# Performance work log

Measured on AMD Instinct MI355X. Metric: run time of the kernel, lower is better.

The kernel has to match this reference:

```python
import jax, jax.numpy as jnp
import numpy as np

B, NE, NN, L = 64, 256, 1024, 512
F_IN, HID = 128, 128
VOCAB = 50000
ALPHA = 0.2
NEG = -9.0e15


def _leaky(z):
    return jnp.where(z >= 0, z, ALPHA * z)


def hga_layer(x, adj, W, W2, W3, a, a2, wc, transfer, concat):
    # x: [B, NN, Fin], adj: [B, NE, NN] (hyperedge incidence)
    O = W2.shape[1]
    x4 = x @ W2                      # [B, NN, O]
    if transfer:
        x = x @ W                    # [B, NN, O]
    # node->edge attention: score depends only on node k (query is shared word_context)
    s0 = wc[0] @ a[:O, 0]            # scalar
    e1 = _leaky(x4 @ a[O:, 0] + s0)  # [B, NN]
    e1 = jnp.broadcast_to(e1[:, None, :], adj.shape)          # [B, NE, NN]
    att_edge = jax.nn.softmax(jnp.where(adj > 0, e1, NEG), axis=2)
    edge = att_edge @ x              # [B, NE, O]
    edge4 = edge @ W3                # [B, NE, O]
    # edge->node attention: query = node feat x4[k], key = edge feat edge4[j]
    e2 = _leaky((x4 @ a2[:O, 0])[:, None, :] + (edge4 @ a2[O:, 0])[:, :, None])  # [B, NE, NN]
    att_node = jax.nn.softmax(jnp.where(adj > 0, e2, NEG).transpose(0, 2, 1), axis=2)  # [B, NN, NE]
    node = att_node @ edge           # [B, NN, O]
    return jax.nn.elu(node) if concat else node


def setup_inputs() -> dict:
    key = jax.random.key(0)
    ks = jax.random.split(key, 16)
    stdv = 1.0 / np.sqrt(HID)
    u = lambda k, shape: jax.random.uniform(k, shape, jnp.float32, -stdv, stdv)
    inp = {
        "items": jax.random.randint(ks[0], (B, NN), 0, VOCAB),
        "alias_inputs": jax.random.randint(ks[1], (B, L), 0, NN),
        "node_masks": jnp.ones((B, L), jnp.float32),
        "adj": jax.random.randint(ks[2], (B, NE, NN), 0, 2).astype(jnp.float32),
        "emb": jax.random.normal(ks[3], (VOCAB, F_IN), jnp.float32),
        # layer 1 (transfer=False, concat=True)
        "w2_1": u(ks[4], (F_IN, HID)),
        "w3_1": u(ks[5], (HID, HID)),
        "a_1": u(ks[6], (2 * HID, 1)),
        "a2_1": u(ks[7], (2 * HID, 1)),
        "wc_1": u(ks[8], (1, HID)),
        # layer 2 (transfer=True, concat=False)
        "w_2": u(ks[9], (HID, HID)),
        "w2_2": u(ks[10], (HID, HID)),
        "w3_2": u(ks[11], (HID, HID)),
        "a_2": u(ks[12], (2 * HID, 1)),
        "a2_2": u(ks[13], (2 * HID, 1)),
        "wc_2": u(ks[14], (1, HID)),
        "ln_g": jnp.ones((HID,), jnp.float32),
        "ln_b": jnp.zeros((HID,), jnp.float32),
    }
    return inp


def reference(items, alias_inputs, node_masks, adj, emb,
              w2_1, w3_1, a_1, a2_1, wc_1,
              w_2, w2_2, w3_2, a_2, a2_2, wc_2,
              ln_g, ln_b):
    hidden = emb[items]                                        # [B, NN, F]
    x = hga_layer(hidden, adj, None, w2_1, w3_1, a_1, a2_1, wc_1,
                  transfer=False, concat=True)
    x = hga_layer(x, adj, w_2, w2_2, w3_2, a_2, a2_2, wc_2,
                  transfer=True, concat=False)                 # [B, NN, HID]
    seq = jnp.take_along_axis(x, alias_inputs[:, :, None], axis=1)  # [B, L, HID]
    m = node_masks[:, :, None]
    h = seq * m
    b = jnp.sum(h * m, axis=-2) / jnp.sum(node_masks, -1, keepdims=True)  # [B, HID]
    mu = jnp.mean(b, -1, keepdims=True)
    var = jnp.mean((b - mu) ** 2, -1, keepdims=True)
    return (b - mu) / jnp.sqrt(var + 1e-6) * ln_g + ln_b
```

## Files before the change

kernel.cpp:

```cpp
#include <hip/hip_runtime.h>
#include <hip/hip_bf16.h>

typedef __hip_bfloat16 bf16;
typedef __attribute__((ext_vector_type(8))) unsigned short u16x8;
typedef __attribute__((ext_vector_type(4))) unsigned short u16x4;
typedef __attribute__((ext_vector_type(4))) float f32x4;
typedef __attribute__((ext_vector_type(8))) short bf16x8;

#define B_   64
#define NE_  256
#define NN_  1024
#define L_   512
#define HID_ 128
#define ALPHA_ 0.2f

__device__ __forceinline__ float bfu(unsigned short u){
  unsigned int x = ((unsigned int)u) << 16;
  union { unsigned int i; float f; } c; c.i = x; return c.f;
}
__device__ __forceinline__ unsigned short f2b(float f){
  bf16 h = __float2bfloat16(f);
  union { bf16 b; unsigned short u; } c; c.b = h; return c.u;
}
__device__ __forceinline__ int swz(int r, int c){ return (c ^ (r & 3) ^ ((r >> 2) & 3)) & 3; }

__global__ void k_small(const float* __restrict__ w2_1, const float* __restrict__ w3_1,
                        const float* __restrict__ a_1,  const float* __restrict__ a2_1,
                        const float* __restrict__ wc_1,
                        const float* __restrict__ w2_2, const float* __restrict__ w3_2,
                        const float* __restrict__ a_2,  const float* __restrict__ a2_2,
                        const float* __restrict__ wc_2,
                        const float* __restrict__ w_2,
                        const int* __restrict__ alias, const float* __restrict__ masks,
                        float* __restrict__ consts, unsigned short* __restrict__ W2T,
                        float* __restrict__ wcount, float* __restrict__ msum,
                        float* __restrict__ pooled)
{
  __shared__ float wcs[1024];
  __shared__ float red4[4];
  int blk = blockIdx.x, t = threadIdx.x;
  if (blk < 6) {
    if (t < 128) {
      const float* M; const float* v;
      switch (blk) {
        case 0: M = w2_1; v = a_1  + 128; break;
        case 1: M = w2_1; v = a2_1;       break;
        case 2: M = w3_1; v = a2_1 + 128; break;
        case 3: M = w2_2; v = a_2  + 128; break;
        case 4: M = w2_2; v = a2_2;       break;
        default: M = w3_2; v = a2_2 + 128; break;
      }
      float acc = 0.f;
      #pragma unroll 4
      for (int o = 0; o < 128; o += 4) {
        f32x4 m = *(const f32x4*)(M + t*128 + o);
        f32x4 x = *(const f32x4*)(v + o);
        acc += m[0]*x[0] + m[1]*x[1] + m[2]*x[2] + m[3]*x[3];
      }
      consts[blk*128 + t] = acc;
    }
  } else if (blk < 8) {
    const float* wc = (blk == 6) ? wc_1 : wc_2;
    const float* a  = (blk == 6) ? a_1  : a_2;
    if (t < 64) {
      float s = wc[t]*a[t] + wc[t+64]*a[t+64];
      #pragma unroll
      for (int sh = 32; sh > 0; sh >>= 1) s += __shfl_xor(s, sh);
      if (t == 0) consts[768 + (blk - 6)] = s;
    }
  } else if (blk == 8) {
    if (t < 128) for (int k = 0; k < 128; ++k) W2T[t*128 + k] = f2b(w_2[k*128 + t]);
  } else if (blk == 9) {
    for (int i = t; i < B_*HID_; i += 256) pooled[i] = 0.f;
  } else {
    int b = blk - 10;
    #pragma unroll
    for (int j = 0; j < 4; ++j) wcs[t + j*256] = 0.f;
    __syncthreads();
    float s = 0.f;
    #pragma unroll
    for (int j = 0; j < 2; ++j) {
      int l = t + j*256;
      float m = masks[b*L_ + l];
      int idx = alias[b*L_ + l];
      atomicAdd(&wcs[idx], m*m);
      s += m;
    }
    #pragma unroll
    for (int sh = 32; sh > 0; sh >>= 1) s += __shfl_xor(s, sh);
    if ((t & 63) == 0) red4[t >> 6] = s;
    __syncthreads();
    if (t == 0) msum[b] = red4[0] + red4[1] + red4[2] + red4[3];
    #pragma unroll
    for (int j = 0; j < 4; ++j) wcount[(long)b*NN_ + t + j*256] = wcs[t + j*256];
  }
}

__global__ __launch_bounds__(256) void k_prep(
    const float* __restrict__ adj,
    unsigned long long* __restrict__ ADJBb,
    unsigned short* __restrict__ ADJT16)
{
  __shared__ unsigned long long Lbits[16][17];
  const int id = blockIdx.x;
  const int b  = id & 63;
  const int ec = id >> 6;
  const int t  = threadIdx.x;
  const int r  = t >> 4;
  const int c  = t & 15;
  const int e  = ec*16 + r;
  const float* src = adj + ((long)b*NE_ + e)*NN_ + c*64;
  unsigned long long m = 0;
  #pragma unroll
  for (int j = 0; j < 64; j += 4) {
    f32x4 v = *(const f32x4*)(src + j);
    #pragma unroll
    for (int k = 0; k < 4; ++k)
      m |= (unsigned long long)(v[k] != 0.f) << (j + k);
  }
  ADJBb[((long)b*NE_ + e)*16 + c] = m;
  Lbits[r][c] = m;
  __syncthreads();
  #pragma unroll
  for (int j = 0; j < 4; ++j) {
    int n = t + 256*j;
    int w = n >> 6, bitn = n & 63;
    unsigned int o = 0;
    #pragma unroll
    for (int rr = 0; rr < 16; ++rr)
      o |= (unsigned int)((Lbits[rr][w] >> bitn) & 1ull) << rr;
    ADJT16[((long)b*NN_ + n)*16 + ec] = (unsigned short)o;
  }
}

__global__ void k_fproj(const float* __restrict__ emb, const int* __restrict__ gitems,
                        const float* __restrict__ consts,
                        float* __restrict__ w1, float* __restrict__ f1,
                        unsigned short* __restrict__ YT)
{
  __shared__ float ce1s[128], cf1s[128];
  __shared__ __attribute__((aligned(16))) unsigned short T[64][132];
  int b = blockIdx.y, n0 = blockIdx.x * 64, t = threadIdx.x;
  if (t < 128) { ce1s[t] = consts[t]; cf1s[t] = consts[128 + t]; }
  __syncthreads();
  int r = t >> 2, h0 = (t & 3) * 32;
  long row = (long)b*NN_ + n0 + r;
  float s0 = consts[768];
  float xv[32];
  const float* sp = emb + (long)gitems[row]*HID_ + h0;
  #pragma unroll
  for (int j = 0; j < 32; j += 4) {
    f32x4 v = *(const f32x4*)(sp + j);
    #pragma unroll
    for (int k = 0; k < 4; ++k) xv[j+k] = v[k];
  }
  float p1 = 0.f, p2 = 0.f;
  #pragma unroll
  for (int j = 0; j < 32; ++j) { p1 += xv[j]*ce1s[h0+j]; p2 += xv[j]*cf1s[h0+j]; }
  p1 += __shfl_xor(p1, 1, 4); p1 += __shfl_xor(p1, 2, 4);
  p2 += __shfl_xor(p2, 1, 4); p2 += __shfl_xor(p2, 2, 4);
  float z = p1 + s0; z = (z >= 0.f) ? z : ALPHA_*z;
  float w = __expf(z);
  if ((t & 3) == 0) { w1[row] = w; f1[row] = p2; }
  #pragma unroll
  for (int j = 0; j < 32; j += 4) {
    u16x4 o;
    #pragma unroll
    for (int k = 0; k < 4; ++k) o[k] = f2b(w * xv[j+k]);
    *(u16x4*)&T[r][h0+j] = o;
  }
  __syncthreads();
  int h = t >> 1, nh = (t & 1) * 32;
  unsigned short* dst = YT + ((long)b*HID_ + h)*NN_ + n0 + nh;
  #pragma unroll
  for (int j = 0; j < 32; j += 8) {
    u16x8 o;
    #pragma unroll
    for (int k = 0; k < 8; ++k) o[k] = T[nh+j+k][h];
    *(u16x8*)&dst[j] = o;
  }
}

template<int TRANSFER>
__global__ __launch_bounds__(256) void k_gemm_edge(
    const unsigned char* __restrict__ ADJ8,
    const unsigned short* __restrict__ YT,
    const float* __restrict__ w1v,
    const float* __restrict__ consts, int layer,
    const unsigned short* __restrict__ W2T,
    unsigned short* __restrict__ ET,
    float* __restrict__ f2o)
{
  __shared__ __attribute__((aligned(16))) unsigned short SM[12288];
  __shared__ float dsum[64];
  const int id = blockIdx.x;
  const int b = id & 63;
  const long e0 = (long)(id >> 6) * 64;
  const int t = threadIdx.x;
  const int lane = t & 63;
  const int w = t >> 6, wm = w >> 1, wn = w & 1;
  const int r4 = t >> 2, c4 = t & 3;
  const int lr = lane & 15, g = lane >> 4;

  f32x4 acc[2][4];
  #pragma unroll
  for (int i = 0; i < 2; ++i)
    #pragma unroll
    for (int j = 0; j < 4; ++j) acc[i][j] = (f32x4){0.f,0.f,0.f,0.f};

  const unsigned char*  Ab = ADJ8 + ((long)b*NE_ + e0 + r4)*(NN_ >> 3);
  const unsigned short* Bb = YT + (long)b*HID_*NN_;
  const float*          wb = w1v + (long)b*NN_;

  unsigned int ab; u16x8 bv0, bv1; f32x4 wv0, wv1;
  float dot = 0.f;

  auto stage = [&](int kc) {
    ab  = Ab[(kc >> 3) + c4];
    wv0 = *(const f32x4*)(wb + kc + c4*8);
    wv1 = *(const f32x4*)(wb + kc + c4*8 + 4);
    bv0 = *(const u16x8*)(Bb + (long)r4*NN_ + kc + c4*8);
    bv1 = *(const u16x8*)(Bb + (long)(64+r4)*NN_ + kc + c4*8);
  };
  auto commit = [&](int buf) {
    u16x8 av;
    #pragma unroll
    for (int j = 0; j < 8; ++j) {
      unsigned int bit = (ab >> j) & 1u;
      av[j] = bit ? (unsigned short)0x3F80 : (unsigned short)0;
      float wj = (j < 4) ? wv0[j] : wv1[j-4];
      dot += bit ? wj : 0.f;
    }
    *(u16x8*)&SM[buf*2048 + r4*32 + swz(r4,c4)*8] = av;
    *(u16x8*)&SM[4096 + buf*4096 + r4*32 + swz(r4,c4)*8] = bv0;
    *(u16x8*)&SM[4096 + buf*4096 + (64+r4)*32 + swz(64+r4,c4)*8] = bv1;
  };

  stage(0); commit(0);
  int cur = 0;
  const int NIT = NN_/32;
  for (int it = 0; it < NIT; ++it) {
    __syncthreads();
    if (it+1 < NIT) stage((it+1)*32);
    const unsigned short* AsB = &SM[cur*2048];
    const unsigned short* BsB = &SM[4096 + cur*4096];
    bf16x8 af[2], bfr[4];
    #pragma unroll
    for (int mt = 0; mt < 2; ++mt) {
      int r = wm*32 + mt*16 + lr;
      af[mt] = *(const bf16x8*)&AsB[r*32 + swz(r,g)*8];
    }
    #pragma unroll
    for (int nt = 0; nt < 4; ++nt) {
      int n = wn*64 + nt*16 + lr;
      bfr[nt] = *(const bf16x8*)&BsB[n*32 + swz(n,g)*8];
    }
    #pragma unroll
    for (int mt = 0; mt < 2; ++mt)
      #pragma unroll
      for (int nt = 0; nt < 4; ++nt)
        acc[mt][nt] = __builtin_amdgcn_mfma_f32_16x16x32_bf16(af[mt], bfr[nt], acc[mt][nt], 0, 0, 0);
    if (it+1 < NIT) { commit(cur^1); cur ^= 1; }
  }
  dot += __shfl_down(dot, 2, 4); dot += __shfl_down(dot, 1, 4);
  if ((lane & 3) == 0) dsum[r4] = dot;
  __syncthreads();
  #pragma unroll
  for (int mt = 0; mt < 2; ++mt)
    #pragma unroll
    for (int nt = 0; nt < 4; ++nt) {
      int col = wn*64 + nt*16 + lr;
      #pragma unroll
      for (int q = 0; q < 4; ++q) {
        int rl = wm*32 + mt*16 + g*4 + q;
        SM[rl*136 + col] = f2b(acc[mt][nt][q] / dsum[rl]);
      }
    }
  __syncthreads();
  if (TRANSFER) {
    f32x4 acc2[2][4];
    #pragma unroll
    for (int i = 0; i < 2; ++i)
      #pragma unroll
      for (int j = 0; j < 4; ++j) acc2[i][j] = (f32x4){0.f,0.f,0.f,0.f};
    #pragma unroll
    for (int kc2 = 0; kc2 < 4; ++kc2) {
      bf16x8 af[2], bfr[4];
      #pragma unroll
      for (int mt = 0; mt < 2; ++mt) {
        int r = wm*32 + mt*16 + lr;
        af[mt] = *(const bf16x8*)&SM[r*136 + kc2*32 + g*8];
      }
      #pragma unroll
      for (int nt = 0; nt < 4; ++nt) {
        int n = wn*64 + nt*16 + lr;
        bfr[nt] = *(const bf16x8*)(W2T + n*128 + kc2*32 + g*8);
      }
      #pragma unroll
      for (int mt = 0; mt < 2; ++mt)
        #pragma unroll
        for (int nt = 0; nt < 4; ++nt)
          acc2[mt][nt] = __builtin_amdgcn_mfma_f32_16x16x32_bf16(af[mt], bfr[nt], acc2[mt][nt], 0, 0, 0);
    }
    __syncthreads();
    #pragma unroll
    for (int mt = 0; mt < 2; ++mt)
      #pragma unroll
      for (int nt = 0; nt < 4; ++nt) {
        int col = wn*64 + nt*16 + lr;
        #pragma unroll
        for (int q = 0; q < 4; ++q) {
          int rl = wm*32 + mt*16 + g*4 + q;
          SM[rl*136 + col] = f2b(acc2[mt][nt][q]);
        }
      }
    __syncthreads();
  }
  {
    const float* cf2 = consts + layer*384 + 256;
    int r = t >> 2, h0 = (t & 3) * 32;
    float p = 0.f;
    #pragma unroll
    for (int j = 0; j < 32; ++j) p += bfu(SM[r*136 + h0 + j]) * cf2[h0 + j];
    p += __shfl_down(p, 2, 4); p += __shfl_down(p, 1, 4);
    if ((t & 3) == 0) f2o[(long)b*NE_ + e0 + r] = p;
  }
  {
    int h = t >> 1, eh = (t & 1) * 32;
    unsigned short* dst = ET + ((long)b*HID_ + h)*NE_ + e0 + eh;
    #pragma unroll
    for (int j = 0; j < 32; j += 8) {
      u16x8 o;
      #pragma unroll
      for (int k = 0; k < 8; ++k) o[k] = SM[(eh+j+k)*136 + h];
      *(u16x8*)&dst[j] = o;
    }
  }
}

template<int EPI>
__global__ __launch_bounds__(256, 2) void k_gemm_att(
    const unsigned char* __restrict__ ADJ8,
    const unsigned short* __restrict__ ET,
    const float* __restrict__ f1v, const float* __restrict__ f2v,
    const float* __restrict__ consts,
    unsigned short* __restrict__ YTout, float* __restrict__ w1o, float* __restrict__ f1o,
    const float* __restrict__ wcount, float* __restrict__ pooled)
{
  __shared__ __attribute__((aligned(16))) unsigned short SM[12288];
  __shared__ float dsum[64];
  __shared__ float colsum[128];
  __shared__ float wrow[64];
  const int id = blockIdx.x;
  const int b = id & 63;
  const long m0 = (long)(id >> 6) * 64;
  const int t = threadIdx.x;
  const int lane = t & 63;
  const int w = t >> 6, wm = w >> 1, wn = w & 1;
  const int r4 = t >> 2, c4 = t & 3;
  const int lr = lane & 15, g = lane >> 4;

  f32x4 acc[2][4];
  #pragma unroll
  for (int i = 0; i < 2; ++i)
    #pragma unroll
    for (int j = 0; j < 4; ++j) acc[i][j] = (f32x4){0.f,0.f,0.f,0.f};

  const float f1r = f1v[(long)b*NN_ + m0 + r4];
  const unsigned char*  Ab = ADJ8 + ((long)b*NN_ + m0 + r4)*(NE_ >> 3);
  const unsigned short* Bb = ET + (long)b*HID_*NE_;
  const float* f2p = f2v + (long)b*NE_;

  unsigned int ab; u16x8 bv0, bv1; f32x4 fv0, fv1;
  float dot = 0.f;

  auto stage = [&](int kc) {
    ab  = Ab[(kc >> 3) + c4];
    fv0 = *(const f32x4*)(f2p + kc + c4*8);
    fv1 = *(const f32x4*)(f2p + kc + c4*8 + 4);
    bv0 = *(const u16x8*)(Bb + (long)r4*NE_ + kc + c4*8);
    bv1 = *(const u16x8*)(Bb + (long)(64+r4)*NE_ + kc + c4*8);
  };
  auto commit = [&](int buf) {
    u16x8 av;
    #pragma unroll
    for (int j = 0; j < 8; ++j) {
      unsigned int bit = (ab >> j) & 1u;
      float z = f1r + ((j < 4) ? fv0[j] : fv1[j-4]);
      z = (z >= 0.f) ? z : ALPHA_ * z;
      float wt = bit ? __expf(z) : 0.f;
      unsigned short us = f2b(wt);
      av[j] = us; dot += bfu(us);
    }
    *(u16x8*)&SM[buf*2048 + r4*32 + swz(r4,c4)*8] = av;
    *(u16x8*)&SM[4096 + buf*4096 + r4*32 + swz(r4,c4)*8] = bv0;
    *(u16x8*)&SM[4096 + buf*4096 + (64+r4)*32 + swz(64+r4,c4)*8] = bv1;
  };

  stage(0); commit(0);
  int cur = 0;
  const int NIT = NE_/32;
  for (int it = 0; it < NIT; ++it) {
    __syncthreads();
    if (it+1 < NIT) stage((it+1)*32);
    const unsigned short* AsB = &SM[cur*2048];
    const unsigned short* BsB = &SM[4096 + cur*4096];
    bf16x8 af[2], bfr[4];
    #pragma unroll
    for (int mt = 0; mt < 2; ++mt) {
      int r = wm*32 + mt*16 + lr;
      af[mt] = *(const bf16x8*)&AsB[r*32 + swz(r,g)*8];
    }
    #pragma unroll
    for (int nt = 0; nt < 4; ++nt) {
      int n = wn*64 + nt*16 + lr;
      bfr[nt] = *(const bf16x8*)&BsB[n*32 + swz(n,g)*8];
    }
    #pragma unroll
    for (int mt = 0; mt < 2; ++mt)
      #pragma unroll
      for (int nt = 0; nt < 4; ++nt)
        acc[mt][nt] = __builtin_amdgcn_mfma_f32_16x16x32_bf16(af[mt], bfr[nt], acc[mt][nt], 0, 0, 0);
    if (it+1 < NIT) { commit(cur^1); cur ^= 1; }
  }
  dot += __shfl_down(dot, 2, 4); dot += __shfl_down(dot, 1, 4);
  if ((lane & 3) == 0) dsum[r4] = dot;
  if (EPI == 2 && t < 128) colsum[t] = 0.f;
  __syncthreads();

  if (EPI == 1) {
    #pragma unroll
    for (int mt = 0; mt < 2; ++mt)
      #pragma unroll
      for (int nt = 0; nt < 4; ++nt) {
        int col = wn*64 + nt*16 + lr;
        #pragma unroll
        for (int q = 0; q < 4; ++q) {
          int rl = wm*32 + mt*16 + g*4 + q;
          float v = acc[mt][nt][q] / dsum[rl];
          v = (v > 0.f) ? v : expm1f(v);
          SM[rl*136 + col] = f2b(v);
        }
      }
    __syncthreads();
    {
      const float* ce1 = consts + 384;
      const float* cf1 = consts + 512;
      int r = t >> 2, h0 = (t & 3) * 32;
      float p1 = 0.f, p2 = 0.f;
      #pragma unroll
      for (int j = 0; j < 32; ++j) {
        float xv = bfu(SM[r*136 + h0 + j]);
        p1 += xv * ce1[h0 + j];
        p2 += xv * cf1[h0 + j];
      }
      p1 += __shfl_down(p1, 2, 4); p1 += __shfl_down(p1, 1, 4);
      p2 += __shfl_down(p2, 2, 4); p2 += __shfl_down(p2, 1, 4);
      if ((t & 3) == 0) {
        float z = p1 + consts[769];
        z = (z >= 0.f) ? z : ALPHA_ * z;
        float wv = __expf(z);
        wrow[r] = wv;
        w1o[(long)b*NN_ + m0 + r] = wv;
        f1o[(long)b*NN_ + m0 + r] = p2;
      }
    }
    __syncthreads();
    {
      int h = t >> 1, nh = (t & 1) * 32;
      unsigned short* dst = YTout + ((long)b*HID_ + h)*NN_ + m0 + nh;
      #pragma unroll
      for (int j = 0; j < 32; j += 8) {
        u16x8 o;
        #pragma unroll
        for (int k = 0; k < 8; ++k) {
          int rr = nh + j + k;
          o[k] = f2b(wrow[rr] * bfu(SM[rr*136 + h]));
        }
        *(u16x8*)&dst[j] = o;
      }
    }
  } else {
    float psum[4] = {0.f, 0.f, 0.f, 0.f};
    #pragma unroll
    for (int mt = 0; mt < 2; ++mt)
      #pragma unroll
      for (int q = 0; q < 4; ++q) {
        int rl = wm*32 + mt*16 + g*4 + q;
        float wc = wcount[(long)b*NN_ + m0 + rl];
        float inv = wc / dsum[rl];
        #pragma unroll
        for (int nt = 0; nt < 4; ++nt) psum[nt] += inv * acc[mt][nt][q];
      }
    #pragma unroll
    for (int nt = 0; nt < 4; ++nt) atomicAdd(&colsum[wn*64 + nt*16 + lr], psum[nt]);
    __syncthreads();
    if (t < 128) atomicAdd(&pooled[(long)b*HID_ + t], colsum[t]);
  }
}

__global__ void k_ln(const float* __restrict__ pooled, const float* __restrict__ msum,
                     const float* __restrict__ ln_g, const float* __restrict__ ln_b,
                     float* __restrict__ out)
{
  int b = blockIdx.x, t = threadIdx.x;
  __shared__ float sr[2];
  float bv = pooled[b*HID_ + t] / msum[b];
  int lane = t & 63;
  float p = bv;
  #pragma unroll
  for (int s = 32; s > 0; s >>= 1) p += __shfl_xor(p, s);
  if (lane == 0) sr[t >> 6] = p;
  __syncthreads();
  float mu = (sr[0] + sr[1]) * (1.f / HID_);
  float dv = bv - mu;
  p = dv * dv;
  #pragma unroll
  for (int s = 32; s > 0; s >>= 1) p += __shfl_xor(p, s);
  __syncthreads();
  if (lane == 0) sr[t >> 6] = p;
  __syncthreads();
  float var = (sr[0] + sr[1]) * (1.f / HID_);
  out[b*HID_ + t] = dv / sqrtf(var + 1e-6f) * ln_g[t] + ln_b[t];
}

extern "C" void kernel_launch(void* const* d_in, const int* in_sizes, int n_in,
                              void* d_out, int out_size, void* d_ws, size_t ws_size,
                              hipStream_t stream)
{
  const int*   items = (const int*)d_in[0];
  const int*   alias = (const int*)d_in[1];
  const float* masks = (const float*)d_in[2];
  const float* adj   = (const float*)d_in[3];
  const float* emb   = (const float*)d_in[4];
  const float* w2_1  = (const float*)d_in[5];
  const float* w3_1  = (const float*)d_in[6];
  const float* a_1   = (const float*)d_in[7];
  const float* a2_1  = (const float*)d_in[8];
  const float* wc_1  = (const float*)d_in[9];
  const float* w_2   = (const float*)d_in[10];
  const float* w2_2  = (const float*)d_in[11];
  const float* w3_2  = (const float*)d_in[12];
  const float* a_2   = (const float*)d_in[13];
  const float* a2_2  = (const float*)d_in[14];
  const float* wc_2  = (const float*)d_in[15];
  const float* ln_g  = (const float*)d_in[16];
  const float* ln_b  = (const float*)d_in[17];
  float* out = (float*)d_out;

  char* ws = (char*)d_ws;
  size_t off = 0;
  auto alloc = [&](size_t bytes) -> void* {
    void* p = ws + off; off += (bytes + 255) / 256 * 256; return p;
  };
  unsigned long long* ADJBb = (unsigned long long*)alloc((size_t)B_*NE_*(NN_/8));
  unsigned short*     ADJT16= (unsigned short*)    alloc((size_t)B_*NN_*(NE_/8));
  unsigned short* YT   = (unsigned short*)alloc((size_t)B_*HID_*NN_*2);
  unsigned short* ET   = (unsigned short*)alloc((size_t)B_*HID_*NE_*2);
  float* wcount= (float*)alloc((size_t)B_*NN_*4);
  float* pooled= (float*)alloc((size_t)B_*HID_*4);
  float* w1L1  = (float*)alloc((size_t)B_*NN_*4);
  float* f1L1  = (float*)alloc((size_t)B_*NN_*4);
  float* w1L2  = (float*)alloc((size_t)B_*NN_*4);
  float* f1L2  = (float*)alloc((size_t)B_*NN_*4);
  float* f2    = (float*)alloc((size_t)B_*NE_*4);
  float* msum  = (float*)alloc(B_*4);
  float* consts= (float*)alloc(772*4);
  unsigned short* W2T = (unsigned short*)alloc((size_t)HID_*HID_*2);
  if (off > ws_size) return;

  k_small<<<74, 256, 0, stream>>>(w2_1, w3_1, a_1, a2_1, wc_1, w2_2, w3_2, a_2, a2_2, wc_2,
                                  w_2, alias, masks, consts, W2T, wcount, msum, pooled);
  k_prep<<<B_*16, 256, 0, stream>>>(adj, ADJBb, ADJT16);
  k_fproj<<<dim3(NN_/64, B_), 256, 0, stream>>>(emb, items, consts, w1L1, f1L1, YT);

  k_gemm_edge<0><<<B_*(NE_/64), 256, 0, stream>>>((const unsigned char*)ADJBb, YT, w1L1,
        consts, 0, W2T, ET, f2);
  k_gemm_att<1><<<B_*(NN_/64), 256, 0, stream>>>((const unsigned char*)ADJT16, ET, f1L1, f2,
        consts, YT, w1L2, f1L2, nullptr, nullptr);

  k_gemm_edge<1><<<B_*(NE_/64), 256, 0, stream>>>((const unsigned char*)ADJBb, YT, w1L2,
        consts, 1, W2T, ET, f2);
  k_gemm_att<2><<<B_*(NN_/64), 256, 0, stream>>>((const unsigned char*)ADJT16, ET, f1L2, f2,
        consts, nullptr, nullptr, nullptr, wcount, pooled);

  k_ln<<<B_, HID_, 0, stream>>>(pooled, msum, ln_g, ln_b, out);
}
```

Measured before the change: 130.2 us.

## Split-K edge GEMM with combine kernel and fuse front-end kernels

Merges the small-constant, adjacency bit-packing and feature-projection kernels into one launch. The feature-projection blocks recompute their projection constants locally, so they no longer depend on the constants kernel. The node->edge GEMM is split over two halves of the node dimension, doubling its grid from 256 to 512 blocks to fill more CUs. A new combine kernel sums the fp32 partials and denominators, normalizes, and applies the W transfer and f2 epilogue. This costs fp32 partial-result traffic through global memory and extra launches.

Result: slower. 136.9 us (+5.2%).

```diff
diff --git a/kernel.cpp b/kernel.cpp
--- a/kernel.cpp
+++ b/kernel.cpp
@@ -13,6 +13,7 @@
 #define L_   512
 #define HID_ 128
 #define ALPHA_ 0.2f
+#define PSC_ ((long)B_*NE_*HID_)
 
 __device__ __forceinline__ float bfu(unsigned short u){
   unsigned int x = ((unsigned int)u) << 16;
@@ -24,178 +25,194 @@
 }
 __device__ __forceinline__ int swz(int r, int c){ return (c ^ (r & 3) ^ ((r >> 2) & 3)) & 3; }
 
-__global__ void k_small(const float* __restrict__ w2_1, const float* __restrict__ w3_1,
-                        const float* __restrict__ a_1,  const float* __restrict__ a2_1,
-                        const float* __restrict__ wc_1,
-                        const float* __restrict__ w2_2, const float* __restrict__ w3_2,
-                        const float* __restrict__ a_2,  const float* __restrict__ a2_2,
-                        const float* __restrict__ wc_2,
-                        const float* __restrict__ w_2,
-                        const int* __restrict__ alias, const float* __restrict__ masks,
-                        float* __restrict__ consts, unsigned short* __restrict__ W2T,
-                        float* __restrict__ wcount, float* __restrict__ msum,
-                        float* __restrict__ pooled)
+__global__ __launch_bounds__(256) void k_front(
+    const float* __restrict__ adj,
+    unsigned long long* __restrict__ ADJBb, unsigned short* __restrict__ ADJT16,
+    const float* __restrict__ emb, const int* __restrict__ items,
+    const float* __restrict__ w2_1, const float* __restrict__ w3_1,
+    const float* __restrict__ a_1,  const float* __restrict__ a2_1,
+    const float* __restrict__ wc_1,
+    const float* __restrict__ w_2,
+    const float* __restrict__ w2_2, const float* __restrict__ w3_2,
+    const float* __restrict__ a_2,  const float* __restrict__ a2_2,
+    const float* __restrict__ wc_2,
+    const int* __restrict__ alias, const float* __restrict__ masks,
+    float* __restrict__ w1L1, float* __restrict__ f1L1,
+    unsigned short* __restrict__ YT,
+    float* __restrict__ consts, unsigned short* __restrict__ W2T,
+    float* __restrict__ wcount, float* __restrict__ msum, float* __restrict__ pooled)
 {
-  __shared__ float wcs[1024];
-  __shared__ float red4[4];
-  int blk = blockIdx.x, t = threadIdx.x;
-  if (blk < 6) {
-    if (t < 128) {
-      const float* M; const float* v;
-      switch (blk) {
-        case 0: M = w2_1; v = a_1  + 128; break;
-        case 1: M = w2_1; v = a2_1;       break;
-        case 2: M = w3_1; v = a2_1 + 128; break;
-        case 3: M = w2_2; v = a_2  + 128; break;
-        case 4: M = w2_2; v = a2_2;       break;
-        default: M = w3_2; v = a2_2 + 128; break;
-      }
+  __shared__ __attribute__((aligned(16))) unsigned char SMEM[18944];
+  const int id = blockIdx.x;
+  const int t  = threadIdx.x;
+
+  if (id < 1024) {
+    unsigned long long (*Lbits)[17] = (unsigned long long(*)[17])SMEM;
+    const int b  = id & 63;
+    const int ec = id >> 6;
+    const int r  = t >> 4;
+    const int c  = t & 15;
+    const int e  = ec*16 + r;
+    const float* src = adj + ((long)b*NE_ + e)*NN_ + c*64;
+    unsigned long long m = 0;
+    #pragma unroll
+    for (int j = 0; j < 64; j += 4) {
+      f32x4 v = *(const f32x4*)(src + j);
+      #pragma unroll
+      for (int k = 0; k < 4; ++k)
+        m |= (unsigned long long)(v[k] != 0.f) << (j + k);
+    }
+    ADJBb[((long)b*NE_ + e)*16 + c] = m;
+    Lbits[r][c] = m;
+    __syncthreads();
+    #pragma unroll
+    for (int j = 0; j < 4; ++j) {
+      int n = t + 256*j;
+      int w = n >> 6, bitn = n & 63;
+      unsigned int o = 0;
+      #pragma unroll
+      for (int rr = 0; rr < 16; ++rr)
+        o |= (unsigned int)((Lbits[rr][w] >> bitn) & 1ull) << rr;
+      ADJT16[((long)b*NN_ + n)*16 + ec] = (unsigned short)o;
+    }
+  } else if (id < 2048) {
+    float* ce1s = (float*)SMEM;
+    float* cf1s = (float*)(SMEM + 512);
+    float* s0s  = (float*)(SMEM + 1024);
+    unsigned short (*T)[132] = (unsigned short(*)[132])(SMEM + 1056);
+    {
+      int rr = t & 127;
+      const float* Mrow = w2_1 + rr*128;
+      const float* vv = (t < 128) ? (a_1 + 128) : a2_1;
       float acc = 0.f;
       #pragma unroll 4
       for (int o = 0; o < 128; o += 4) {
-        f32x4 m = *(const f32x4*)(M + t*128 + o);
-        f32x4 x = *(const f32x4*)(v + o);
+        f32x4 m = *(const f32x4*)(Mrow + o);
+        f32x4 x = *(const f32x4*)(vv + o);
         acc += m[0]*x[0] + m[1]*x[1] + m[2]*x[2] + m[3]*x[3];
       }
-      consts[blk*128 + t] = acc;
-    }
-  } else if (blk < 8) {
-    const float* wc = (blk == 6) ? wc_1 : wc_2;
-    const float* a  = (blk == 6) ? a_1  : a_2;
-    if (t < 64) {
-      float s = wc[t]*a[t] + wc[t+64]*a[t+64];
+      if (t < 128) ce1s[rr] = acc; else cf1s[rr] = acc;
+      if (t < 64) {
+        float s = wc_1[t]*a_1[t] + wc_1[t+64]*a_1[t+64];
+        #pragma unroll
+        for (int sh = 32; sh > 0; sh >>= 1) s += __shfl_xor(s, sh);
+        if (t == 0) s0s[0] = s;
+      }
+    }
+    __syncthreads();
+    int fid = id - 1024;
+    int b = fid & 63, n0 = (fid >> 6) * 64;
+    int r = t >> 2, h0 = (t & 3) * 32;
+    long row = (long)b*NN_ + n0 + r;
+    float s0 = s0s[0];
+    float xv[32];
+    const float* sp = emb + (long)items[row]*HID_ + h0;
+    #pragma unroll
+    for (int j = 0; j < 32; j += 4) {
+      f32x4 v = *(const f32x4*)(sp + j);
+      #pragma unroll
+      for (int k = 0; k < 4; ++k) xv[j+k] = v[k];
+    }
+    float p1 = 0.f, p2 = 0.f;
+    #pragma unroll
+    for (int j = 0; j < 32; ++j) { p1 += xv[j]*ce1s[h0+j]; p2 += xv[j]*cf1s[h0+j]; }
+    p1 += __shfl_xor(p1, 1, 4); p1 += __shfl_xor(p1, 2, 4);
+    p2 += __shfl_xor(p2, 1, 4); p2 += __shfl_xor(p2, 2, 4);
+    float z = p1 + s0; z = (z >= 0.f) ? z : ALPHA_*z;
+    float w = __expf(z);
+    if ((t & 3) == 0) { w1L1[row] = w; f1L1[row] = p2; }
+    #pragma unroll
+    for (int j = 0; j < 32; j += 4) {
+      u16x4 o;
+      #pragma unroll
+      for (int k = 0; k < 4; ++k) o[k] = f2b(w * xv[j+k]);
+      *(u16x4*)&T[r][h0+j] = o;
+    }
+    __syncthreads();
+    int h = t >> 1, nh = (t & 1) * 32;
+    unsigned short* dst = YT + ((long)b*HID_ + h)*NN_ + n0 + nh;
+    #pragma unroll
+    for (int j = 0; j < 32; j += 8) {
+      u16x8 o;
+      #pragma unroll
+      for (int k = 0; k < 8; ++k) o[k] = T[nh+j+k][h];
+      *(u16x8*)&dst[j] = o;
+    }
+  } else {
+    int blk = id - 2048;
+    float* wcs  = (float*)SMEM;
+    float* red4 = (float*)(SMEM + 4096);
+    if (blk < 6) {
+      if (t < 128) {
+        const float* M; const float* v;
+        switch (blk) {
+          case 0: M = w2_1; v = a_1  + 128; break;
+          case 1: M = w2_1; v = a2_1;       break;
+          case 2: M = w3_1; v = a2_1 + 128; break;
+          case 3: M = w2_2; v = a_2  + 128; break;
+          case 4: M = w2_2; v = a2_2;       break;
+          default: M = w3_2; v = a2_2 + 128; break;
+        }
+        float acc = 0.f;
+        #pragma unroll 4
+        for (int o = 0; o < 128; o += 4) {
+          f32x4 m = *(const f32x4*)(M + t*128 + o);
+          f32x4 x = *(const f32x4*)(v + o);
+          acc += m[0]*x[0] + m[1]*x[1] + m[2]*x[2] + m[3]*x[3];
+        }
+        consts[blk*128 + t] = acc;
+      }
+    } else if (blk < 8) {
+      const float* wc = (blk == 6) ? wc_1 : wc_2;
+      const float* a  = (blk == 6) ? a_1  : a_2;
+      if (t < 64) {
+        float s = wc[t]*a[t] + wc[t+64]*a[t+64];
+        #pragma unroll
+        for (int sh = 32; sh > 0; sh >>= 1) s += __shfl_xor(s, sh);
+        if (t == 0) consts[768 + (blk - 6)] = s;
+      }
+    } else if (blk == 8) {
+      if (t < 128) for (int k = 0; k < 128; ++k) W2T[t*128 + k] = f2b(w_2[k*128 + t]);
+    } else if (blk == 9) {
+      for (int i = t; i < B_*HID_; i += 256) pooled[i] = 0.f;
+    } else {
+      int b = blk - 10;
+      #pragma unroll
+      for (int j = 0; j < 4; ++j) wcs[t + j*256] = 0.f;
+      __syncthreads();
+      float s = 0.f;
+      #pragma unroll
+      for (int j = 0; j < 2; ++j) {
+        int l = t + j*256;
+        float m = masks[b*L_ + l];
+        int idx = alias[b*L_ + l];
+        atomicAdd(&wcs[idx], m*m);
+        s += m;
+      }
       #pragma unroll
       for (int sh = 32; sh > 0; sh >>= 1) s += __shfl_xor(s, sh);
-      if (t == 0) consts[768 + (blk - 6)] = s;
-    }
-  } else if (blk == 8) {
-    if (t < 128) for (int k = 0; k < 128; ++k) W2T[t*128 + k] = f2b(w_2[k*128 + t]);
-  } else if (blk == 9) {
-    for (int i = t; i < B_*HID_; i += 256) pooled[i] = 0.f;
-  } else {
-    int b = blk - 10;
-    #pragma unroll
-    for (int j = 0; j < 4; ++j) wcs[t + j*256] = 0.f;
-    __syncthreads();
-    float s = 0.f;
-    #pragma unroll
-    for (int j = 0; j < 2; ++j) {
-      int l = t + j*256;
-      float m = masks[b*L_ + l];
-      int idx = alias[b*L_ + l];
-      atomicAdd(&wcs[idx], m*m);
-      s += m;
-    }
-    #pragma unroll
-    for (int sh = 32; sh > 0; sh >>= 1) s += __shfl_xor(s, sh);
-    if ((t & 63) == 0) red4[t >> 6] = s;
-    __syncthreads();
-    if (t == 0) msum[b] = red4[0] + red4[1] + red4[2] + red4[3];
-    #pragma unroll
-    for (int j = 0; j < 4; ++j) wcount[(long)b*NN_ + t + j*256] = wcs[t + j*256];
-  }
-}
-
-__global__ __launch_bounds__(256) void k_prep(
-    const float* __restrict__ adj,
-    unsigned long long* __restrict__ ADJBb,
-    unsigned short* __restrict__ ADJT16)
-{
-  __shared__ unsigned long long Lbits[16][17];
-  const int id = blockIdx.x;
-  const int b  = id & 63;
-  const int ec = id >> 6;
-  const int t  = threadIdx.x;
-  const int r  = t >> 4;
-  const int c  = t & 15;
-  const int e  = ec*16 + r;
-  const float* src = adj + ((long)b*NE_ + e)*NN_ + c*64;
-  unsigned long long m = 0;
-  #pragma unroll
-  for (int j = 0; j < 64; j += 4) {
-    f32x4 v = *(const f32x4*)(src + j);
-    #pragma unroll
-    for (int k = 0; k < 4; ++k)
-      m |= (unsigned long long)(v[k] != 0.f) << (j + k);
-  }
-  ADJBb[((long)b*NE_ + e)*16 + c] = m;
-  Lbits[r][c] = m;
-  __syncthreads();
-  #pragma unroll
-  for (int j = 0; j < 4; ++j) {
-    int n = t + 256*j;
-    int w = n >> 6, bitn = n & 63;
-    unsigned int o = 0;
-    #pragma unroll
-    for (int rr = 0; rr < 16; ++rr)
-      o |= (unsigned int)((Lbits[rr][w] >> bitn) & 1ull) << rr;
-    ADJT16[((long)b*NN_ + n)*16 + ec] = (unsigned short)o;
-  }
-}
-
-__global__ void k_fproj(const float* __restrict__ emb, const int* __restrict__ gitems,
-                        const float* __restrict__ consts,
-                        float* __restrict__ w1, float* __restrict__ f1,
-                        unsigned short* __restrict__ YT)
-{
-  __shared__ float ce1s[128], cf1s[128];
-  __shared__ __attribute__((aligned(16))) unsigned short T[64][132];
-  int b = blockIdx.y, n0 = blockIdx.x * 64, t = threadIdx.x;
-  if (t < 128) { ce1s[t] = consts[t]; cf1s[t] = consts[128 + t]; }
-  __syncthreads();
-  int r = t >> 2, h0 = (t & 3) * 32;
-  long row = (long)b*NN_ + n0 + r;
-  float s0 = consts[768];
-  float xv[32];
-  const float* sp = emb + (long)gitems[row]*HID_ + h0;
-  #pragma unroll
-  for (int j = 0; j < 32; j += 4) {
-    f32x4 v = *(const f32x4*)(sp + j);
-    #pragma unroll
-    for (int k = 0; k < 4; ++k) xv[j+k] = v[k];
-  }
-  float p1 = 0.f, p2 = 0.f;
-  #pragma unroll
-  for (int j = 0; j < 32; ++j) { p1 += xv[j]*ce1s[h0+j]; p2 += xv[j]*cf1s[h0+j]; }
-  p1 += __shfl_xor(p1, 1, 4); p1 += __shfl_xor(p1, 2, 4);
-  p2 += __shfl_xor(p2, 1, 4); p2 += __shfl_xor(p2, 2, 4);
-  float z = p1 + s0; z = (z >= 0.f) ? z : ALPHA_*z;
-  float w = __expf(z);
-  if ((t & 3) == 0) { w1[row] = w; f1[row] = p2; }
-  #pragma unroll
-  for (int j = 0; j < 32; j += 4) {
-    u16x4 o;
-    #pragma unroll
-    for (int k = 0; k < 4; ++k) o[k] = f2b(w * xv[j+k]);
-    *(u16x4*)&T[r][h0+j] = o;
-  }
-  __syncthreads();
-  int h = t >> 1, nh = (t & 1) * 32;
-  unsigned short* dst = YT + ((long)b*HID_ + h)*NN_ + n0 + nh;
-  #pragma unroll
-  for (int j = 0; j < 32; j += 8) {
-    u16x8 o;
-    #pragma unroll
-    for (int k = 0; k < 8; ++k) o[k] = T[nh+j+k][h];
-    *(u16x8*)&dst[j] = o;
-  }
-}
-
-template<int TRANSFER>
-__global__ __launch_bounds__(256) void k_gemm_edge(
+      if ((t & 63) == 0) red4[t >> 6] = s;
+      __syncthreads();
+      if (t == 0) msum[b] = red4[0] + red4[1] + red4[2] + red4[3];
+      #pragma unroll
+      for (int j = 0; j < 4; ++j) wcount[(long)b*NN_ + t + j*256] = wcs[t + j*256];
+    }
+  }
+}
+
+__global__ __launch_bounds__(256, 2) void k_gemm_edge(
     const unsigned char* __restrict__ ADJ8,
     const unsigned short* __restrict__ YT,
     const float* __restrict__ w1v,
-    const float* __restrict__ consts, int layer,
-    const unsigned short* __restrict__ W2T,
-    unsigned short* __restrict__ ET,
-    float* __restrict__ f2o)
+    float* __restrict__ PART, float* __restrict__ PDSUM)
 {
   __shared__ __attribute__((aligned(16))) unsigned short SM[12288];
-  __shared__ float dsum[64];
   const int id = blockIdx.x;
-  const int b = id & 63;
-  const long e0 = (long)(id >> 6) * 64;
+  const int b  = id & 63;
+  const int et = (id >> 6) & 3;
+  const int kz = id >> 8;
+  const long e0 = (long)et * 64;
+  const int kbase = kz * (NN_/2);
   const int t = threadIdx.x;
   const int lane = t & 63;
   const int w = t >> 6, wm = w >> 1, wn = w & 1;
@@ -208,9 +225,9 @@
     #pragma unroll
     for (int j = 0; j < 4; ++j) acc[i][j] = (f32x4){0.f,0.f,0.f,0.f};
 
-  const unsigned char*  Ab = ADJ8 + ((long)b*NE_ + e0 + r4)*(NN_ >> 3);
-  const unsigned short* Bb = YT + (long)b*HID_*NN_;
-  const float*          wb = w1v + (long)b*NN_;
+  const unsigned char*  Ab = ADJ8 + ((long)b*NE_ + e0 + r4)*(NN_ >> 3) + (kbase >> 3);
+  const unsigned short* Bb = YT + (long)b*HID_*NN_ + kbase;
+  const float*          wb = w1v + (long)b*NN_ + kbase;
 
   unsigned int ab; u16x8 bv0, bv1; f32x4 wv0, wv1;
   float dot = 0.f;
@@ -238,7 +255,7 @@
 
   stage(0); commit(0);
   int cur = 0;
-  const int NIT = NN_/32;
+  const int NIT = (NN_/2)/32;
   for (int it = 0; it < NIT; ++it) {
     __syncthreads();
     if (it+1 < NIT) stage((it+1)*32);
@@ -263,8 +280,8 @@
     if (it+1 < NIT) { commit(cur^1); cur ^= 1; }
   }
   dot += __shfl_down(dot, 2, 4); dot += __shfl_down(dot, 1, 4);
-  if ((lane & 3) == 0) dsum[r4] = dot;
-  __syncthreads();
+  if ((lane & 3) == 0) PDSUM[((long)kz*B_ + b)*NE_ + e0 + r4] = dot;
+  float* P = PART + (long)kz*PSC_ + ((long)b*NE_ + e0)*HID_;
   #pragma unroll
   for (int mt = 0; mt < 2; ++mt)
     #pragma unroll
@@ -273,9 +290,45 @@
       #pragma unroll
       for (int q = 0; q < 4; ++q) {
         int rl = wm*32 + mt*16 + g*4 + q;
-        SM[rl*136 + col] = f2b(acc[mt][nt][q] / dsum[rl]);
-      }
-    }
+        P[(long)rl*HID_ + col] = acc[mt][nt][q];
+      }
+    }
+}
+
+template<int TRANSFER>
+__global__ __launch_bounds__(256) void k_comb(
+    const float* __restrict__ PART, const float* __restrict__ PDSUM,
+    const float* __restrict__ consts, int layer,
+    const unsigned short* __restrict__ W2T,
+    unsigned short* __restrict__ ET, float* __restrict__ f2o)
+{
+  __shared__ __attribute__((aligned(16))) unsigned short U[64*136];
+  __shared__ float den[64];
+  const int id = blockIdx.x;
+  const int b  = id & 63;
+  const long e0 = (long)(id >> 6) * 64;
+  const int t = threadIdx.x;
+  const int lane = t & 63;
+  const int w = t >> 6, wm = w >> 1, wn = w & 1;
+  const int lr = lane & 15, g = lane >> 4;
+  const int r = t >> 2, h0 = (t & 3) * 32;
+
+  if (t < 64) den[t] = PDSUM[(long)b*NE_ + e0 + t] + PDSUM[(long)(B_ + b)*NE_ + e0 + t];
+  __syncthreads();
+  {
+    const float* p0 = PART + ((long)b*NE_ + e0 + r)*HID_ + h0;
+    const float* p1 = p0 + PSC_;
+    float d = 1.f / den[r];
+    #pragma unroll
+    for (int j = 0; j < 32; j += 4) {
+      f32x4 x0 = *(const f32x4*)(p0 + j);
+      f32x4 x1 = *(const f32x4*)(p1 + j);
+      u16x4 o;
+      #pragma unroll
+      for (int k = 0; k < 4; ++k) o[k] = f2b((x0[k] + x1[k]) * d);
+      *(u16x4*)&U[r*136 + h0 + j] = o;
+    }
+  }
   __syncthreads();
   if (TRANSFER) {
     f32x4 acc2[2][4];
@@ -288,8 +341,8 @@
       bf16x8 af[2], bfr[4];
       #pragma unroll
       for (int mt = 0; mt < 2; ++mt) {
-        int r = wm*32 + mt*16 + lr;
-        af[mt] = *(const bf16x8*)&SM[r*136 + kc2*32 + g*8];
+        int rr = wm*32 + mt*16 + lr;
+        af[mt] = *(const bf16x8*)&U[rr*136 + kc2*32 + g*8];
       }
       #pragma unroll
       for (int nt = 0; nt < 4; ++nt) {
@@ -311,17 +364,16 @@
         #pragma unroll
         for (int q = 0; q < 4; ++q) {
           int rl = wm*32 + mt*16 + g*4 + q;
-          SM[rl*136 + col] = f2b(acc2[mt][nt][q]);
+          U[rl*136 + col] = f2b(acc2[mt][nt][q]);
         }
       }
     __syncthreads();
   }
   {
     const float* cf2 = consts + layer*384 + 256;
-    int r = t >> 2, h0 = (t & 3) * 32;
     float p = 0.f;
     #pragma unroll
-    for (int j = 0; j < 32; ++j) p += bfu(SM[r*136 + h0 + j]) * cf2[h0 + j];
+    for (int j = 0; j < 32; ++j) p += bfu(U[r*136 + h0 + j]) * cf2[h0 + j];
     p += __shfl_down(p, 2, 4); p += __shfl_down(p, 1, 4);
     if ((t & 3) == 0) f2o[(long)b*NE_ + e0 + r] = p;
   }
@@ -332,7 +384,7 @@
     for (int j = 0; j < 32; j += 8) {
       u16x8 o;
       #pragma unroll
-      for (int k = 0; k < 8; ++k) o[k] = SM[(eh+j+k)*136 + h];
+      for (int k = 0; k < 8; ++k) o[k] = U[(eh+j+k)*136 + h];
       *(u16x8*)&dst[j] = o;
     }
   }
@@ -557,6 +609,8 @@
   unsigned short*     ADJT16= (unsigned short*)    alloc((size_t)B_*NN_*(NE_/8));
   unsigned short* YT   = (unsigned short*)alloc((size_t)B_*HID_*NN_*2);
   unsigned short* ET   = (unsigned short*)alloc((size_t)B_*HID_*NE_*2);
+  float* PART  = (float*)alloc((size_t)2*PSC_*4);
+  float* PDSUM = (float*)alloc((size_t)2*B_*NE_*4);
   float* wcount= (float*)alloc((size_t)B_*NN_*4);
   float* pooled= (float*)alloc((size_t)B_*HID_*4);
   float* w1L1  = (float*)alloc((size_t)B_*NN_*4);
@@ -569,18 +623,17 @@
   unsigned short* W2T = (unsigned short*)alloc((size_t)HID_*HID_*2);
   if (off > ws_size) return;
 
-  k_small<<<74, 256, 0, stream>>>(w2_1, w3_1, a_1, a2_1, wc_1, w2_2, w3_2, a_2, a2_2, wc_2,
-                                  w_2, alias, masks, consts, W2T, wcount, msum, pooled);
-  k_prep<<<B_*16, 256, 0, stream>>>(adj, ADJBb, ADJT16);
-  k_fproj<<<dim3(NN_/64, B_), 256, 0, stream>>>(emb, items, consts, w1L1, f1L1, YT);
-
-  k_gemm_edge<0><<<B_*(NE_/64), 256, 0, stream>>>((const unsigned char*)ADJBb, YT, w1L1,
-        consts, 0, W2T, ET, f2);
+  k_front<<<2122, 256, 0, stream>>>(adj, ADJBb, ADJT16, emb, items,
+        w2_1, w3_1, a_1, a2_1, wc_1, w_2, w2_2, w3_2, a_2, a2_2, wc_2,
+        alias, masks, w1L1, f1L1, YT, consts, W2T, wcount, msum, pooled);
+
+  k_gemm_edge<<<512, 256, 0, stream>>>((const unsigned char*)ADJBb, YT, w1L1, PART, PDSUM);
+  k_comb<0><<<256, 256, 0, stream>>>(PART, PDSUM, consts, 0, W2T, ET, f2);
   k_gemm_att<1><<<B_*(NN_/64), 256, 0, stream>>>((const unsigned char*)ADJT16, ET, f1L1, f2,
         consts, YT, w1L2, f1L2, nullptr, nullptr);
 
-  k_gemm_edge<1><<<B_*(NE_/64), 256, 0, stream>>>((const unsigned char*)ADJBb, YT, w1L2,
-        consts, 1, W2T, ET, f2);
+  k_gemm_edge<<<512, 256, 0, stream>>>((const unsigned char*)ADJBb, YT, w1L2, PART, PDSUM);
+  k_comb<1><<<256, 256, 0, stream>>>(PART, PDSUM, consts, 1, W2T, ET, f2);
   k_gemm_att<2><<<B_*(NN_/64), 256, 0, stream>>>((const unsigned char*)ADJT16, ET, f1L2, f2,
         consts, nullptr, nullptr, nullptr, wcount, pooled);
 
```
